# Optimization experiments

Hardware: AMD Instinct MI355X
Metric: run time of the kernel (lower is better)

## Reference

```python
import jax, jax.numpy as jnp
import numpy as np

B, L, D, DK, T = 8192, 64, 512, 64, 128
WIDE_IN = 2 * T + T * T  # 16640


def setup_inputs() -> dict:
    key = jax.random.key(0)
    ks = jax.random.split(key, 24)
    s = 0.02
    inp = {
        "mashup_tags": jax.random.uniform(ks[0], (B, T), jnp.float32),
        "target_api_tags": jax.random.uniform(ks[1], (B, T), jnp.float32),
        "cross_product_tag": jax.random.uniform(ks[2], (B, T * T), jnp.float32),
        "encoded_api_context": jax.random.normal(ks[3], (B, L, D), jnp.float32),
        "candidate_api_description_feature": jax.random.normal(ks[4], (B, D), jnp.float32),
        "mashup_description_feature": jax.random.normal(ks[5], (B, D), jnp.float32),
        "context_len": jax.random.randint(ks[6], (B,), 0, L + 1, jnp.int64 if jax.config.jax_enable_x64 else jnp.int32),
        # attention projections (torch Linear weight layout: [out, in], no bias)
        "W_K": s * jax.random.normal(ks[7], (DK, D), jnp.float32),
        "W_Q": s * jax.random.normal(ks[8], (DK, D), jnp.float32),
        # wide head
        "wide_w": s * jax.random.normal(ks[9], (1, WIDE_IN), jnp.float32),
        "wide_b": jnp.zeros((1,), jnp.float32),
        # deep MLP 1536->512->256->128->1
        "d1_w": s * jax.random.normal(ks[10], (512, 3 * D), jnp.float32),
        "d1_b": jnp.zeros((512,), jnp.float32),
        "d2_w": s * jax.random.normal(ks[11], (256, 512), jnp.float32),
        "d2_b": jnp.zeros((256,), jnp.float32),
        "d3_w": s * jax.random.normal(ks[12], (128, 256), jnp.float32),
        "d3_b": jnp.zeros((128,), jnp.float32),
        "d4_w": s * jax.random.normal(ks[13], (1, 128), jnp.float32),
        "d4_b": jnp.zeros((1,), jnp.float32),
        "wide_weight": jnp.ones((1,), jnp.float32),
        "deep_weight": jnp.ones((1,), jnp.float32),
        "bias": jnp.zeros((1,), jnp.float32),
    }
    return inp


def reference(mashup_tags, target_api_tags, cross_product_tag,
              encoded_api_context, candidate_api_description_feature,
              mashup_description_feature, context_len,
              W_K, W_Q, wide_w, wide_b,
              d1_w, d1_b, d2_w, d2_b, d3_w, d3_b, d4_w, d4_b,
              wide_weight, deep_weight, bias):
    # ---- wide branch ----
    wide_in = jnp.concatenate([mashup_tags, target_api_tags, cross_product_tag], axis=1)
    wide_out = jax.nn.sigmoid(wide_in @ wide_w.T + wide_b)  # (B,1)

    # ---- ragged attention (vectorized masked softmax replaces the Python batch loop) ----
    K = jnp.einsum("bld,kd->blk", encoded_api_context, W_K)          # (B,L,dk)
    Q = candidate_api_description_feature @ W_Q.T                     # (B,dk)
    scores = jnp.einsum("blk,bk->bl", K, Q)                           # (B,L)
    mask = jnp.arange(scores.shape[1])[None, :] < context_len[:, None]
    m = jnp.max(jnp.where(mask, scores, -1e30), axis=-1, keepdims=True)
    e = jnp.where(mask, jnp.exp(scores - m), 0.0)
    denom = jnp.sum(e, axis=-1, keepdims=True)
    probs = e / jnp.maximum(denom, 1e-30)  # rows with length==0 -> all zeros (matches torch zeros fallback)
    api_context = jnp.einsum("bl,bld->bd", probs, encoded_api_context)  # (B,512)

    # ---- deep branch ----
    deep_in = jnp.concatenate([mashup_description_feature, api_context,
                               candidate_api_description_feature], axis=1)  # (B,1536)
    h = jax.nn.relu(deep_in @ d1_w.T + d1_b)
    h = jax.nn.relu(h @ d2_w.T + d2_b)
    h = jax.nn.relu(h @ d3_w.T + d3_b)
    deep_out = h @ d4_w.T + d4_b  # (B,1)

    out = wide_weight * wide_out + deep_weight * deep_out + bias
    return jax.nn.sigmoid(out)
```

## Files before the change

kernel.cpp:

```cpp
#include <hip/hip_runtime.h>

#define Bsz 8192
#define Lctx 64
#define Ddim 512
#define DK 64
#define Ttag 128
#define RQT 4

using f32x4 = __attribute__((ext_vector_type(4))) float;
using bf16x8 = __attribute__((ext_vector_type(8))) short;

__device__ __forceinline__ float wave_sum(float v) {
#pragma unroll
    for (int m = 32; m > 0; m >>= 1) v += __shfl_xor(v, m, 64);
    return v;
}

__device__ __forceinline__ float dot4(float4 a, float4 b) {
    return a.x * b.x + a.y * b.y + a.z * b.z + a.w * b.w;
}

__device__ __forceinline__ unsigned f2bf(float f) {
    unsigned int u = __float_as_uint(f);
    u = u + 0x7fffu + ((u >> 16) & 1u);
    return u >> 16;
}
__device__ __forceinline__ unsigned pack2(float a, float b) {
    return f2bf(a) | (f2bf(b) << 16);
}
__device__ __forceinline__ float bf2f(unsigned short u) { return __uint_as_float((unsigned)u << 16); }

__global__ __launch_bounds__(256) void k_f2bf3(
    const float* __restrict__ s1, unsigned short* __restrict__ d1,
    const float* __restrict__ s2, unsigned short* __restrict__ d2,
    const float* __restrict__ s3, unsigned short* __restrict__ d3)
{
    int i = blockIdx.x * 256 + threadIdx.x;
    const float* s;
    unsigned short* d;
    if (i < 196608)      { s = s1; d = d1; }
    else if (i < 229376) { i -= 196608; s = s2; d = d2; }
    else if (i < 237568) { i -= 229376; s = s3; d = d3; }
    else return;
    const float4 v = ((const float4*)s)[i];
    uint2 w;
    w.x = pack2(v.x, v.y);
    w.y = pack2(v.z, v.w);
    *(uint2*)&d[(size_t)i * 4] = w;
}

__global__ __launch_bounds__(256) void k_qtilde(
    const float* __restrict__ C, const float* __restrict__ WQ,
    const float* __restrict__ WK, float* __restrict__ qt)
{
    const int lane = threadIdx.x & 63;
    const int gw = blockIdx.x * 4 + (threadIdx.x >> 6);
    const int b0 = gw * RQT;

    float4 c0[RQT], c1[RQT];
#pragma unroll
    for (int r = 0; r < RQT; ++r) {
        const float4* row = (const float4*)(C + (size_t)(b0 + r) * Ddim);
        c0[r] = row[lane];
        c1[r] = row[64 + lane];
    }
    float tv[RQT];
#pragma unroll
    for (int r = 0; r < RQT; ++r) tv[r] = 0.f;
    for (int k = 0; k < DK; ++k) {
        const float4* wrow = (const float4*)(WQ + (size_t)k * Ddim);
        const float4 w0 = wrow[lane];
        const float4 w1 = wrow[64 + lane];
#pragma unroll
        for (int r = 0; r < RQT; ++r) {
            float p = dot4(c0[r], w0) + dot4(c1[r], w1);
            p = wave_sum(p);
            if (lane == k) tv[r] = p;
        }
    }
    float4 a0[RQT], a1[RQT];
#pragma unroll
    for (int r = 0; r < RQT; ++r) {
        a0[r] = make_float4(0.f, 0.f, 0.f, 0.f);
        a1[r] = make_float4(0.f, 0.f, 0.f, 0.f);
    }
    for (int k = 0; k < DK; ++k) {
        const float4* wrow = (const float4*)(WK + (size_t)k * Ddim);
        const float4 w0 = wrow[lane];
        const float4 w1 = wrow[64 + lane];
#pragma unroll
        for (int r = 0; r < RQT; ++r) {
            const float tk = __shfl(tv[r], k, 64);
            a0[r].x += tk * w0.x; a0[r].y += tk * w0.y;
            a0[r].z += tk * w0.z; a0[r].w += tk * w0.w;
            a1[r].x += tk * w1.x; a1[r].y += tk * w1.y;
            a1[r].z += tk * w1.z; a1[r].w += tk * w1.w;
        }
    }
#pragma unroll
    for (int r = 0; r < RQT; ++r) {
        float4* orow = (float4*)(qt + (size_t)(b0 + r) * Ddim);
        orow[lane] = a0[r];
        orow[64 + lane] = a1[r];
    }
}

__global__ __launch_bounds__(256, 4) void k_attn_wide(
    const float* __restrict__ X, const float* __restrict__ qt,
    const int* __restrict__ clen, const float* __restrict__ mdesc,
    const float* __restrict__ cand,
    const float* __restrict__ mt, const float* __restrict__ tt,
    const float* __restrict__ cp, const float* __restrict__ ww,
    const float* __restrict__ wb,
    unsigned short* __restrict__ din, float* __restrict__ wl)
{
    const int tid = threadIdx.x;
    const int wave = tid >> 6, lane = tid & 63;
    const int b = blockIdx.x * 4 + wave;
    const int len = clen[b];

    const float4* qrow = (const float4*)(qt + (size_t)b * Ddim);
    const float4 q0 = qrow[lane];
    const float4 q1 = qrow[64 + lane];
    const float4* xb = (const float4*)(X + (size_t)b * Lctx * Ddim);

    float4 y0 = make_float4(0.f, 0.f, 0.f, 0.f);
    float4 y1 = make_float4(0.f, 0.f, 0.f, 0.f);
    float M = -1e30f, D = 0.f;

    const int nch = (len + 7) >> 3;
    for (int c = 0; c < nch; ++c) {
        const int base = c * 8;
        const int nr = min(8, len - base);
        float4 t0[8], t1[8];
#pragma unroll
        for (int r = 0; r < 8; ++r) {
            const int l = base + min(r, nr - 1);
            t0[r] = xb[l * 128 + lane];
            t1[r] = xb[l * 128 + 64 + lane];
        }
        float sc[8];
#pragma unroll
        for (int r = 0; r < 8; ++r)
            sc[r] = dot4(t0[r], q0) + dot4(t1[r], q1);
#pragma unroll
        for (int r = 0; r < 8; ++r) sc[r] = wave_sum(sc[r]);

        float pmax = -1e30f;
#pragma unroll
        for (int r = 0; r < 8; ++r)
            if (r < nr) pmax = fmaxf(pmax, sc[r]);
        const float Mn = fmaxf(M, pmax);
        const float scale = __expf(M - Mn);
        D *= scale;
        y0.x *= scale; y0.y *= scale; y0.z *= scale; y0.w *= scale;
        y1.x *= scale; y1.y *= scale; y1.z *= scale; y1.w *= scale;
#pragma unroll
        for (int r = 0; r < 8; ++r) {
            if (r < nr) {
                const float e = __expf(sc[r] - Mn);
                D += e;
                y0.x += e * t0[r].x; y0.y += e * t0[r].y;
                y0.z += e * t0[r].z; y0.w += e * t0[r].w;
                y1.x += e * t1[r].x; y1.y += e * t1[r].y;
                y1.z += e * t1[r].z; y1.w += e * t1[r].w;
            }
        }
        M = Mn;
    }

    float wacc;
    {
        const float2 a  = ((const float2*)(mt + (size_t)b * Ttag))[lane];
        const float2 wA = ((const float2*)ww)[lane];
        const float2 t  = ((const float2*)(tt + (size_t)b * Ttag))[lane];
        const float2 wB = ((const float2*)(ww + Ttag))[lane];
        wacc = a.x * wA.x + a.y * wA.y + t.x * wB.x + t.y * wB.y;
    }
    {
        const float4* cp4 = (const float4*)(cp + (size_t)b * (Ttag * Ttag));
        const float4* ww4 = (const float4*)(ww + 2 * Ttag);
        float wa = 0.f, wbk = 0.f;
#pragma unroll 8
        for (int i = 0; i < 64; i += 2) {
            wa  += dot4(cp4[i * 64 + lane],       ww4[i * 64 + lane]);
            wbk += dot4(cp4[(i + 1) * 64 + lane], ww4[(i + 1) * 64 + lane]);
        }
        wacc += wa + wbk;
    }
    wacc = wave_sum(wacc);
    if (lane == 0) wl[b] = wacc + wb[0];

    unsigned short* dr = din + (size_t)b * 1536;
    const float rden = 1.f / fmaxf(D, 1e-30f);
    {
        uint2 w;
        w.x = pack2(y0.x * rden, y0.y * rden);
        w.y = pack2(y0.z * rden, y0.w * rden);
        *(uint2*)&dr[512 + 4 * lane] = w;
        w.x = pack2(y1.x * rden, y1.y * rden);
        w.y = pack2(y1.z * rden, y1.w * rden);
        *(uint2*)&dr[512 + 256 + 4 * lane] = w;
    }
    {
        const float4* md = (const float4*)(mdesc + (size_t)b * Ddim);
        const float4 m0 = md[lane], m1 = md[64 + lane];
        uint2 w;
        w.x = pack2(m0.x, m0.y); w.y = pack2(m0.z, m0.w);
        *(uint2*)&dr[4 * lane] = w;
        w.x = pack2(m1.x, m1.y); w.y = pack2(m1.z, m1.w);
        *(uint2*)&dr[256 + 4 * lane] = w;
    }
    {
        const float4* cd = (const float4*)(cand + (size_t)b * Ddim);
        const float4 c0 = cd[lane], c1 = cd[64 + lane];
        uint2 w;
        w.x = pack2(c0.x, c0.y); w.y = pack2(c0.z, c0.w);
        *(uint2*)&dr[1024 + 4 * lane] = w;
        w.x = pack2(c1.x, c1.y); w.y = pack2(c1.z, c1.w);
        *(uint2*)&dr[1024 + 256 + 4 * lane] = w;
    }
}

__global__ __launch_bounds__(256) void k_gemm_bf16(
    const unsigned short* __restrict__ A, const unsigned short* __restrict__ W,
    const float* __restrict__ bias, unsigned short* __restrict__ C,
    const int K, const int N, const int relu)
{
    __shared__ unsigned short As[128][72];
    __shared__ unsigned short Bs[128][72];
    const int tid = threadIdx.x;
    const int wave = tid >> 6, lane = tid & 63;
    const int wm = wave >> 1, wn = wave & 1;
    const size_t m0 = (size_t)blockIdx.x * 128;
    const size_t n0 = (size_t)blockIdx.y * 128;

    f32x4 acc[4][4];
#pragma unroll
    for (int i = 0; i < 4; ++i)
#pragma unroll
        for (int j = 0; j < 4; ++j) acc[i][j] = (f32x4){0.f, 0.f, 0.f, 0.f};

    uint4 pa[4], pb[4];
    auto loadA = [&](int k0) {
#pragma unroll
        for (int j = 0; j < 4; ++j) {
            const int i = tid + j * 256;
            const int row = i >> 3, c8 = (i & 7) * 8;
            pa[j] = *(const uint4*)(A + (m0 + row) * (size_t)K + k0 + c8);
        }
    };
    auto loadB = [&](int k0) {
#pragma unroll
        for (int j = 0; j < 4; ++j) {
            const int i = tid + j * 256;
            const int row = i >> 3, c8 = (i & 7) * 8;
            pb[j] = *(const uint4*)(W + (n0 + row) * (size_t)K + k0 + c8);
        }
    };

    loadA(0);
    loadB(0);
    for (int k0 = 0; k0 < K; k0 += 64) {
        __syncthreads();
#pragma unroll
        for (int j = 0; j < 4; ++j) {
            const int i = tid + j * 256;
            const int row = i >> 3, c8 = (i & 7) * 8;
            *(uint4*)&As[row][c8] = pa[j];
            *(uint4*)&Bs[row][c8] = pb[j];
        }
        __syncthreads();
        if (k0 + 64 < K) { loadA(k0 + 64); loadB(k0 + 64); }
#pragma unroll
        for (int kk = 0; kk < 2; ++kk) {
            const int krow = kk * 32 + (lane >> 4) * 8;
            bf16x8 af[4], bfr[4];
#pragma unroll
            for (int mm = 0; mm < 4; ++mm)
                af[mm] = *(const bf16x8*)&As[wm * 64 + mm * 16 + (lane & 15)][krow];
#pragma unroll
            for (int nn = 0; nn < 4; ++nn)
                bfr[nn] = *(const bf16x8*)&Bs[wn * 64 + nn * 16 + (lane & 15)][krow];
#pragma unroll
            for (int mm = 0; mm < 4; ++mm)
#pragma unroll
                for (int nn = 0; nn < 4; ++nn)
                    acc[mm][nn] = __builtin_amdgcn_mfma_f32_16x16x32_bf16(
                        af[mm], bfr[nn], acc[mm][nn], 0, 0, 0);
        }
    }

#pragma unroll
    for (int nn = 0; nn < 4; ++nn) {
        const int col = (int)n0 + wn * 64 + nn * 16 + (lane & 15);
        const float bv = bias[col];
#pragma unroll
        for (int mm = 0; mm < 4; ++mm) {
#pragma unroll
            for (int r = 0; r < 4; ++r) {
                const size_t row = m0 + wm * 64 + mm * 16 + (lane >> 4) * 4 + r;
                float v = acc[mm][nn][r] + bv;
                if (relu) v = fmaxf(v, 0.f);
                C[row * N + col] = (unsigned short)f2bf(v);
            }
        }
    }
}

__global__ __launch_bounds__(256) void k_final(
    const unsigned short* __restrict__ h3, const float* __restrict__ d4w,
    const float* __restrict__ d4b, const float* __restrict__ wl,
    const float* __restrict__ wwt, const float* __restrict__ dwt,
    const float* __restrict__ bs, float* __restrict__ out)
{
    const int lane = threadIdx.x & 63;
    const int b = blockIdx.x * 4 + (threadIdx.x >> 6);
    const unsigned short* hr = h3 + (size_t)b * 128;
    float v = bf2f(hr[lane]) * d4w[lane] + bf2f(hr[64 + lane]) * d4w[64 + lane];
    v = wave_sum(v);
    if (lane == 0) {
        const float deep = v + d4b[0];
        const float wo = 1.f / (1.f + __expf(-wl[b]));
        const float z = wwt[0] * wo + dwt[0] * deep + bs[0];
        out[b] = 1.f / (1.f + __expf(-z));
    }
}

extern "C" void kernel_launch(void* const* d_in, const int* in_sizes, int n_in,
                              void* d_out, int out_size, void* d_ws, size_t ws_size,
                              hipStream_t stream)
{
    const float* mt    = (const float*)d_in[0];
    const float* tt    = (const float*)d_in[1];
    const float* cp    = (const float*)d_in[2];
    const float* X     = (const float*)d_in[3];
    const float* cand  = (const float*)d_in[4];
    const float* mdesc = (const float*)d_in[5];
    const int*   clen  = (const int*)d_in[6];
    const float* WK    = (const float*)d_in[7];
    const float* WQ    = (const float*)d_in[8];
    const float* ww    = (const float*)d_in[9];
    const float* wb    = (const float*)d_in[10];
    const float* d1w   = (const float*)d_in[11];
    const float* d1b   = (const float*)d_in[12];
    const float* d2w   = (const float*)d_in[13];
    const float* d2b   = (const float*)d_in[14];
    const float* d3w   = (const float*)d_in[15];
    const float* d3b   = (const float*)d_in[16];
    const float* d4w   = (const float*)d_in[17];
    const float* d4b   = (const float*)d_in[18];
    const float* wwt   = (const float*)d_in[19];
    const float* dwt   = (const float*)d_in[20];
    const float* bs    = (const float*)d_in[21];
    float* out = (float*)d_out;

    char* w = (char*)d_ws;
    unsigned short* din = (unsigned short*)w;            w += (size_t)Bsz * 1536 * 2;
    float* qt           = (float*)w;                     w += (size_t)Bsz * 512 * 4;
    unsigned short* h1  = (unsigned short*)w;            w += (size_t)Bsz * 512 * 2;
    unsigned short* h2  = (unsigned short*)w;            w += (size_t)Bsz * 256 * 2;
    unsigned short* h3  = (unsigned short*)w;            w += (size_t)Bsz * 128 * 2;
    float* wl           = (float*)w;                     w += (size_t)Bsz * 4;
    unsigned short* w1b = (unsigned short*)w;            w += (size_t)512 * 1536 * 2;
    unsigned short* w2b = (unsigned short*)w;            w += (size_t)256 * 512 * 2;
    unsigned short* w3b = (unsigned short*)w;            w += (size_t)128 * 256 * 2;

    hipLaunchKernelGGL(k_f2bf3, dim3(928), dim3(256), 0, stream,
                       d1w, w1b, d2w, w2b, d3w, w3b);
    hipLaunchKernelGGL(k_qtilde, dim3(Bsz / (RQT * 4)), dim3(256), 0, stream,
                       cand, WQ, WK, qt);
    hipLaunchKernelGGL(k_attn_wide, dim3(Bsz / 4), dim3(256), 0, stream,
                       X, qt, clen, mdesc, cand, mt, tt, cp, ww, wb, din, wl);
    hipLaunchKernelGGL(k_gemm_bf16, dim3(64, 4), dim3(256), 0, stream,
                       din, w1b, d1b, h1, 1536, 512, 1);
    hipLaunchKernelGGL(k_gemm_bf16, dim3(64, 2), dim3(256), 0, stream,
                       h1, w2b, d2b, h2, 512, 256, 1);
    hipLaunchKernelGGL(k_gemm_bf16, dim3(64, 1), dim3(256), 0, stream,
                       h2, w3b, d3b, h3, 256, 128, 1);
    hipLaunchKernelGGL(k_final, dim3(Bsz / 4), dim3(256), 0, stream,
                       h3, d4w, d4b, wl, wwt, dwt, bs, out);
}
```

Before: 438.5 us.

## Merge prep kernels, split wide branch into separate blocks, retile GEMMs, fuse final layer

Merges the weight bf16 conversion and q-tilde projection into one launch. The attention kernel's wide-branch dot product moves into separate interleaved blocks so the cross-product stream and the attention stream run in parallel across CUs, and score dot products are skipped for padded rows. The first two GEMMs use a narrower N tile (64) so more blocks launch. The third GEMM is fused with the final 128->1 projection and sigmoid, which removes the h3 buffer and one launch. The risks are a lower arithmetic intensity per GEMM tile and some imbalance between the two block types in the big kernel.

Result: no change. 445.9 us (+1.7%).

```diff
diff --git a/kernel.cpp b/kernel.cpp
--- a/kernel.cpp
+++ b/kernel.cpp
@@ -28,31 +28,29 @@
 __device__ __forceinline__ unsigned pack2(float a, float b) {
     return f2bf(a) | (f2bf(b) << 16);
 }
-__device__ __forceinline__ float bf2f(unsigned short u) { return __uint_as_float((unsigned)u << 16); }
-
-__global__ __launch_bounds__(256) void k_f2bf3(
+
+__global__ __launch_bounds__(256) void k_prep(
+    const float* __restrict__ C, const float* __restrict__ WQ,
+    const float* __restrict__ WK, float* __restrict__ qt,
     const float* __restrict__ s1, unsigned short* __restrict__ d1,
     const float* __restrict__ s2, unsigned short* __restrict__ d2,
     const float* __restrict__ s3, unsigned short* __restrict__ d3)
 {
-    int i = blockIdx.x * 256 + threadIdx.x;
-    const float* s;
-    unsigned short* d;
-    if (i < 196608)      { s = s1; d = d1; }
-    else if (i < 229376) { i -= 196608; s = s2; d = d2; }
-    else if (i < 237568) { i -= 229376; s = s3; d = d3; }
-    else return;
-    const float4 v = ((const float4*)s)[i];
-    uint2 w;
-    w.x = pack2(v.x, v.y);
-    w.y = pack2(v.z, v.w);
-    *(uint2*)&d[(size_t)i * 4] = w;
-}
-
-__global__ __launch_bounds__(256) void k_qtilde(
-    const float* __restrict__ C, const float* __restrict__ WQ,
-    const float* __restrict__ WK, float* __restrict__ qt)
-{
+    if (blockIdx.x >= 512) {
+        int i = (blockIdx.x - 512) * 256 + threadIdx.x;
+        const float* s;
+        unsigned short* d;
+        if (i < 196608)      { s = s1; d = d1; }
+        else if (i < 229376) { i -= 196608; s = s2; d = d2; }
+        else                 { i -= 229376; s = s3; d = d3; }
+        const float4 v = ((const float4*)s)[i];
+        uint2 w;
+        w.x = pack2(v.x, v.y);
+        w.y = pack2(v.z, v.w);
+        *(uint2*)&d[(size_t)i * 4] = w;
+        return;
+    }
+
     const int lane = threadIdx.x & 63;
     const int gw = blockIdx.x * 4 + (threadIdx.x >> 6);
     const int b0 = gw * RQT;
@@ -105,7 +103,7 @@
     }
 }
 
-__global__ __launch_bounds__(256, 4) void k_attn_wide(
+__global__ __launch_bounds__(256) void k_big(
     const float* __restrict__ X, const float* __restrict__ qt,
     const int* __restrict__ clen, const float* __restrict__ mdesc,
     const float* __restrict__ cand,
@@ -114,11 +112,37 @@
     const float* __restrict__ wb,
     unsigned short* __restrict__ din, float* __restrict__ wl)
 {
+    const int g = blockIdx.x;
+    const int kind = (g >> 3) & 1;
+    const int idx = (int)(((g >> 4) << 3) | (g & 7));
     const int tid = threadIdx.x;
     const int wave = tid >> 6, lane = tid & 63;
-    const int b = blockIdx.x * 4 + wave;
+    const int b = idx * 4 + wave;
+
+    if (kind == 1) {
+        float wacc;
+        {
+            const float2 a  = ((const float2*)(mt + (size_t)b * Ttag))[lane];
+            const float2 wA = ((const float2*)ww)[lane];
+            const float2 t  = ((const float2*)(tt + (size_t)b * Ttag))[lane];
+            const float2 wB = ((const float2*)(ww + Ttag))[lane];
+            wacc = a.x * wA.x + a.y * wA.y + t.x * wB.x + t.y * wB.y;
+        }
+        const float4* cp4 = (const float4*)(cp + (size_t)b * (Ttag * Ttag));
+        const float4* ww4 = (const float4*)(ww + 2 * Ttag);
+        float w0 = 0.f, w1 = 0.f;
+#pragma unroll 8
+        for (int i = 0; i < 64; i += 2) {
+            w0 += dot4(cp4[i * 64 + lane],       ww4[i * 64 + lane]);
+            w1 += dot4(cp4[(i + 1) * 64 + lane], ww4[(i + 1) * 64 + lane]);
+        }
+        wacc += w0 + w1;
+        wacc = wave_sum(wacc);
+        if (lane == 0) wl[b] = wacc + wb[0];
+        return;
+    }
+
     const int len = clen[b];
-
     const float4* qrow = (const float4*)(qt + (size_t)b * Ddim);
     const float4 q0 = qrow[lane];
     const float4 q1 = qrow[64 + lane];
@@ -142,9 +166,10 @@
         float sc[8];
 #pragma unroll
         for (int r = 0; r < 8; ++r)
-            sc[r] = dot4(t0[r], q0) + dot4(t1[r], q1);
-#pragma unroll
-        for (int r = 0; r < 8; ++r) sc[r] = wave_sum(sc[r]);
+            if (r < nr) sc[r] = dot4(t0[r], q0) + dot4(t1[r], q1);
+#pragma unroll
+        for (int r = 0; r < 8; ++r)
+            if (r < nr) sc[r] = wave_sum(sc[r]);
 
         float pmax = -1e30f;
 #pragma unroll
@@ -168,28 +193,6 @@
         }
         M = Mn;
     }
-
-    float wacc;
-    {
-        const float2 a  = ((const float2*)(mt + (size_t)b * Ttag))[lane];
-        const float2 wA = ((const float2*)ww)[lane];
-        const float2 t  = ((const float2*)(tt + (size_t)b * Ttag))[lane];
-        const float2 wB = ((const float2*)(ww + Ttag))[lane];
-        wacc = a.x * wA.x + a.y * wA.y + t.x * wB.x + t.y * wB.y;
-    }
-    {
-        const float4* cp4 = (const float4*)(cp + (size_t)b * (Ttag * Ttag));
-        const float4* ww4 = (const float4*)(ww + 2 * Ttag);
-        float wa = 0.f, wbk = 0.f;
-#pragma unroll 8
-        for (int i = 0; i < 64; i += 2) {
-            wa  += dot4(cp4[i * 64 + lane],       ww4[i * 64 + lane]);
-            wbk += dot4(cp4[(i + 1) * 64 + lane], ww4[(i + 1) * 64 + lane]);
-        }
-        wacc += wa + wbk;
-    }
-    wacc = wave_sum(wacc);
-    if (lane == 0) wl[b] = wacc + wb[0];
 
     unsigned short* dr = din + (size_t)b * 1536;
     const float rden = 1.f / fmaxf(D, 1e-30f);
@@ -222,26 +225,30 @@
     }
 }
 
+template <int BN>
 __global__ __launch_bounds__(256) void k_gemm_bf16(
     const unsigned short* __restrict__ A, const unsigned short* __restrict__ W,
     const float* __restrict__ bias, unsigned short* __restrict__ C,
     const int K, const int N, const int relu)
 {
+    constexpr int WN = BN / 2;
+    constexpr int NN = WN / 16;
+    constexpr int NB = (BN * 8) / 256;
     __shared__ unsigned short As[128][72];
-    __shared__ unsigned short Bs[128][72];
+    __shared__ unsigned short Bs[BN][72];
     const int tid = threadIdx.x;
     const int wave = tid >> 6, lane = tid & 63;
     const int wm = wave >> 1, wn = wave & 1;
     const size_t m0 = (size_t)blockIdx.x * 128;
-    const size_t n0 = (size_t)blockIdx.y * 128;
-
-    f32x4 acc[4][4];
+    const size_t n0 = (size_t)blockIdx.y * BN;
+
+    f32x4 acc[4][NN];
 #pragma unroll
     for (int i = 0; i < 4; ++i)
 #pragma unroll
-        for (int j = 0; j < 4; ++j) acc[i][j] = (f32x4){0.f, 0.f, 0.f, 0.f};
-
-    uint4 pa[4], pb[4];
+        for (int j = 0; j < NN; ++j) acc[i][j] = (f32x4){0.f, 0.f, 0.f, 0.f};
+
+    uint4 pa[4], pb[NB];
     auto loadA = [&](int k0) {
 #pragma unroll
         for (int j = 0; j < 4; ++j) {
@@ -252,7 +259,7 @@
     };
     auto loadB = [&](int k0) {
 #pragma unroll
-        for (int j = 0; j < 4; ++j) {
+        for (int j = 0; j < NB; ++j) {
             const int i = tid + j * 256;
             const int row = i >> 3, c8 = (i & 7) * 8;
             pb[j] = *(const uint4*)(W + (n0 + row) * (size_t)K + k0 + c8);
@@ -268,6 +275,11 @@
             const int i = tid + j * 256;
             const int row = i >> 3, c8 = (i & 7) * 8;
             *(uint4*)&As[row][c8] = pa[j];
+        }
+#pragma unroll
+        for (int j = 0; j < NB; ++j) {
+            const int i = tid + j * 256;
+            const int row = i >> 3, c8 = (i & 7) * 8;
             *(uint4*)&Bs[row][c8] = pb[j];
         }
         __syncthreads();
@@ -275,25 +287,25 @@
 #pragma unroll
         for (int kk = 0; kk < 2; ++kk) {
             const int krow = kk * 32 + (lane >> 4) * 8;
-            bf16x8 af[4], bfr[4];
+            bf16x8 af[4], bfr[NN];
 #pragma unroll
             for (int mm = 0; mm < 4; ++mm)
                 af[mm] = *(const bf16x8*)&As[wm * 64 + mm * 16 + (lane & 15)][krow];
 #pragma unroll
-            for (int nn = 0; nn < 4; ++nn)
-                bfr[nn] = *(const bf16x8*)&Bs[wn * 64 + nn * 16 + (lane & 15)][krow];
+            for (int nn = 0; nn < NN; ++nn)
+                bfr[nn] = *(const bf16x8*)&Bs[wn * WN + nn * 16 + (lane & 15)][krow];
 #pragma unroll
             for (int mm = 0; mm < 4; ++mm)
 #pragma unroll
-                for (int nn = 0; nn < 4; ++nn)
+                for (int nn = 0; nn < NN; ++nn)
                     acc[mm][nn] = __builtin_amdgcn_mfma_f32_16x16x32_bf16(
                         af[mm], bfr[nn], acc[mm][nn], 0, 0, 0);
         }
     }
 
 #pragma unroll
-    for (int nn = 0; nn < 4; ++nn) {
-        const int col = (int)n0 + wn * 64 + nn * 16 + (lane & 15);
+    for (int nn = 0; nn < NN; ++nn) {
+        const int col = (int)n0 + wn * WN + nn * 16 + (lane & 15);
         const float bv = bias[col];
 #pragma unroll
         for (int mm = 0; mm < 4; ++mm) {
@@ -308,19 +320,114 @@
     }
 }
 
-__global__ __launch_bounds__(256) void k_final(
-    const unsigned short* __restrict__ h3, const float* __restrict__ d4w,
+__global__ __launch_bounds__(256) void k_gemm3_final(
+    const unsigned short* __restrict__ A, const unsigned short* __restrict__ W,
+    const float* __restrict__ bias, const float* __restrict__ d4w,
     const float* __restrict__ d4b, const float* __restrict__ wl,
     const float* __restrict__ wwt, const float* __restrict__ dwt,
     const float* __restrict__ bs, float* __restrict__ out)
 {
-    const int lane = threadIdx.x & 63;
-    const int b = blockIdx.x * 4 + (threadIdx.x >> 6);
-    const unsigned short* hr = h3 + (size_t)b * 128;
-    float v = bf2f(hr[lane]) * d4w[lane] + bf2f(hr[64 + lane]) * d4w[64 + lane];
-    v = wave_sum(v);
-    if (lane == 0) {
-        const float deep = v + d4b[0];
+    constexpr int K = 256, N = 128;
+    __shared__ unsigned short As[128][72];
+    __shared__ unsigned short Bs[128][72];
+    __shared__ float dp[128][2];
+    const int tid = threadIdx.x;
+    const int wave = tid >> 6, lane = tid & 63;
+    const int wm = wave >> 1, wn = wave & 1;
+    const size_t m0 = (size_t)blockIdx.x * 128;
+
+    f32x4 acc[4][4];
+#pragma unroll
+    for (int i = 0; i < 4; ++i)
+#pragma unroll
+        for (int j = 0; j < 4; ++j) acc[i][j] = (f32x4){0.f, 0.f, 0.f, 0.f};
+
+    uint4 pa[4], pb[4];
+    auto loadA = [&](int k0) {
+#pragma unroll
+        for (int j = 0; j < 4; ++j) {
+            const int i = tid + j * 256;
+            const int row = i >> 3, c8 = (i & 7) * 8;
+            pa[j] = *(const uint4*)(A + (m0 + row) * (size_t)K + k0 + c8);
+        }
+    };
+    auto loadB = [&](int k0) {
+#pragma unroll
+        for (int j = 0; j < 4; ++j) {
+            const int i = tid + j * 256;
+            const int row = i >> 3, c8 = (i & 7) * 8;
+            pb[j] = *(const uint4*)(W + row * (size_t)K + k0 + c8);
+        }
+    };
+
+    loadA(0);
+    loadB(0);
+    for (int k0 = 0; k0 < K; k0 += 64) {
+        __syncthreads();
+#pragma unroll
+        for (int j = 0; j < 4; ++j) {
+            const int i = tid + j * 256;
+            const int row = i >> 3, c8 = (i & 7) * 8;
+            *(uint4*)&As[row][c8] = pa[j];
+            *(uint4*)&Bs[row][c8] = pb[j];
+        }
+        __syncthreads();
+        if (k0 + 64 < K) { loadA(k0 + 64); loadB(k0 + 64); }
+#pragma unroll
+        for (int kk = 0; kk < 2; ++kk) {
+            const int krow = kk * 32 + (lane >> 4) * 8;
+            bf16x8 af[4], bfr[4];
+#pragma unroll
+            for (int mm = 0; mm < 4; ++mm)
+                af[mm] = *(const bf16x8*)&As[wm * 64 + mm * 16 + (lane & 15)][krow];
+#pragma unroll
+            for (int nn = 0; nn < 4; ++nn)
+                bfr[nn] = *(const bf16x8*)&Bs[wn * 64 + nn * 16 + (lane & 15)][krow];
+#pragma unroll
+            for (int mm = 0; mm < 4; ++mm)
+#pragma unroll
+                for (int nn = 0; nn < 4; ++nn)
+                    acc[mm][nn] = __builtin_amdgcn_mfma_f32_16x16x32_bf16(
+                        af[mm], bfr[nn], acc[mm][nn], 0, 0, 0);
+        }
+    }
+
+    float rowpart[4][4];
+#pragma unroll
+    for (int mm = 0; mm < 4; ++mm)
+#pragma unroll
+        for (int r = 0; r < 4; ++r) rowpart[mm][r] = 0.f;
+#pragma unroll
+    for (int nn = 0; nn < 4; ++nn) {
+        const int col = wn * 64 + nn * 16 + (lane & 15);
+        const float bv = bias[col];
+        const float w4 = d4w[col];
+#pragma unroll
+        for (int mm = 0; mm < 4; ++mm)
+#pragma unroll
+            for (int r = 0; r < 4; ++r) {
+                float v = acc[mm][nn][r] + bv;
+                v = fmaxf(v, 0.f);
+                rowpart[mm][r] += v * w4;
+            }
+    }
+#pragma unroll
+    for (int mm = 0; mm < 4; ++mm)
+#pragma unroll
+        for (int r = 0; r < 4; ++r) {
+            float v = rowpart[mm][r];
+            v += __shfl_xor(v, 1, 64);
+            v += __shfl_xor(v, 2, 64);
+            v += __shfl_xor(v, 4, 64);
+            v += __shfl_xor(v, 8, 64);
+            if ((lane & 15) == 0)
+                dp[wm * 64 + mm * 16 + (lane >> 4) * 4 + r][wn] = v;
+        }
+    __syncthreads();
+    if (tid < 128) {
+        const int row = tid;
+        const float deep = dp[row][0] + dp[row][1] + d4b[0];
+        const size_t b = m0 + row;
         const float wo = 1.f / (1.f + __expf(-wl[b]));
         const float z = wwt[0] * wo + dwt[0] * deep + bs[0];
         out[b] = 1.f / (1.f + __expf(-z));
@@ -360,24 +467,19 @@
     float* qt           = (float*)w;                     w += (size_t)Bsz * 512 * 4;
     unsigned short* h1  = (unsigned short*)w;            w += (size_t)Bsz * 512 * 2;
     unsigned short* h2  = (unsigned short*)w;            w += (size_t)Bsz * 256 * 2;
-    unsigned short* h3  = (unsigned short*)w;            w += (size_t)Bsz * 128 * 2;
     float* wl           = (float*)w;                     w += (size_t)Bsz * 4;
     unsigned short* w1b = (unsigned short*)w;            w += (size_t)512 * 1536 * 2;
     unsigned short* w2b = (unsigned short*)w;            w += (size_t)256 * 512 * 2;
     unsigned short* w3b = (unsigned short*)w;            w += (size_t)128 * 256 * 2;
 
-    hipLaunchKernelGGL(k_f2bf3, dim3(928), dim3(256), 0, stream,
-                       d1w, w1b, d2w, w2b, d3w, w3b);
-    hipLaunchKernelGGL(k_qtilde, dim3(Bsz / (RQT * 4)), dim3(256), 0, stream,
-                       cand, WQ, WK, qt);
-    hipLaunchKernelGGL(k_attn_wide, dim3(Bsz / 4), dim3(256), 0, stream,
+    hipLaunchKernelGGL(k_prep, dim3(1440), dim3(256), 0, stream,
+                       cand, WQ, WK, qt, d1w, w1b, d2w, w2b, d3w, w3b);
+    hipLaunchKernelGGL(k_big, dim3(4096), dim3(256), 0, stream,
                        X, qt, clen, mdesc, cand, mt, tt, cp, ww, wb, din, wl);
-    hipLaunchKernelGGL(k_gemm_bf16, dim3(64, 4), dim3(256), 0, stream,
+    hipLaunchKernelGGL((k_gemm_bf16<64>), dim3(64, 8), dim3(256), 0, stream,
                        din, w1b, d1b, h1, 1536, 512, 1);
-    hipLaunchKernelGGL(k_gemm_bf16, dim3(64, 2), dim3(256), 0, stream,
+    hipLaunchKernelGGL((k_gemm_bf16<64>), dim3(64, 4), dim3(256), 0, stream,
                        h1, w2b, d2b, h2, 512, 256, 1);
-    hipLaunchKernelGGL(k_gemm_bf16, dim3(64, 1), dim3(256), 0, stream,
-                       h2, w3b, d3b, h3, 256, 128, 1);
-    hipLaunchKernelGGL(k_final, dim3(Bsz / 4), dim3(256), 0, stream,
-                       h3, d4w, d4b, wl, wwt, dwt, bs, out);
-}
+    hipLaunchKernelGGL(k_gemm3_final, dim3(64), dim3(256), 0, stream,
+                       h2, w3b, d3b, d4w, d4b, wl, wwt, dwt, bs, out);
+}
```
